# Kernel optimization log

Hardware: AMD Instinct MI355X
Metric: run time of the kernel (lower is better)

## Reference

```python
import jax, jax.numpy as jnp
import numpy as np

D_IN = 1024
D_OUT = 1024
H = 16            # head_cnt
G = 4             # attention_groups
LF = 2            # linformer_factor
HEAD_OUT = D_OUT // H          # 64 (value head dim)
DQ = HEAD_OUT // LF            # 32 (query/key head dim)
B, T = 2, 2048


def setup_inputs() -> dict:
    key = jax.random.key(0)
    ks = jax.random.split(key, 7)
    s = 0.02
    return {
        "x": jax.random.normal(ks[0], (B, T, D_IN), dtype=jnp.float32),
        "Wq": jax.random.normal(ks[1], (D_IN, D_OUT // LF), dtype=jnp.float32) * s,
        "Wk": jax.random.normal(ks[2], (D_IN, (D_OUT // LF) // G), dtype=jnp.float32) * s,
        "Wv": jax.random.normal(ks[3], (D_IN, D_OUT // G), dtype=jnp.float32) * s,
        "Wp": jax.random.normal(ks[4], (D_OUT, D_OUT), dtype=jnp.float32) * s,
        "bp": jnp.zeros((D_OUT,), dtype=jnp.float32),
    }


def _alibi_bias(T, dtype):
    # standard ALiBi slopes for H heads (H is a power of 2): m_h = 2^(-8h/H), h=1..H
    slopes = jnp.asarray(2.0 ** (-8.0 * np.arange(1, H + 1) / H), dtype=dtype)
    pos = jnp.arange(T)
    rel = (pos[None, :] - pos[:, None]).astype(dtype)  # j - i, <= 0 on causal part
    return slopes[:, None, None] * rel[None, :, :]      # (H, T, T)


def reference(x, Wq, Wk, Wv, Wp, bp):
    b, t, _ = x.shape
    q = x @ Wq                                  # (b, t, D_OUT/LF)
    k = jnp.tile(x @ Wk, (1, 1, G))             # repeat KV groups -> (b, t, D_OUT/LF)
    v = jnp.tile(x @ Wv, (1, 1, G))             # (b, t, D_OUT)

    q = q.reshape(b, t, H, DQ).transpose(0, 2, 1, 3)        # (b, H, t, DQ)
    k = k.reshape(b, t, H, DQ).transpose(0, 2, 1, 3)
    v = v.reshape(b, t, H, HEAD_OUT).transpose(0, 2, 1, 3)  # (b, H, t, HEAD_OUT)

    scores = jnp.einsum('bhqd,bhkd->bhqk', q, k)            # (b, H, t, t)
    causal = jnp.triu(jnp.ones((t, t), dtype=bool), k=1)
    scores = jnp.where(causal, -jnp.inf, scores)
    # faithful to source: alibi added after masking, then scaled by 1/sqrt(d_k)
    scores = (scores + _alibi_bias(t, scores.dtype)) / jnp.sqrt(jnp.asarray(DQ, scores.dtype))
    w = jax.nn.softmax(scores, axis=-1)
    ctx = jnp.einsum('bhqk,bhkd->bqhd', w, v).reshape(b, t, D_OUT)
    return ctx @ Wp + bp
```

## Files before the change

### kernel.cpp

```cpp
#include <hip/hip_runtime.h>
#include <hip/hip_bf16.h>

#define T_SEQ 2048
#define H_CNT 16
#define B_SZ  2
#define QKV_LD 896
#define KOFF   512
#define VOFF   640

typedef float  f32x4   __attribute__((ext_vector_type(4)));
typedef float  f32x16  __attribute__((ext_vector_type(16)));
typedef __bf16 bf16x8  __attribute__((ext_vector_type(8)));

static __device__ __forceinline__ ushort f2bf(float f) {
    union { float f; unsigned u; } v; v.f = f;
    unsigned u = v.u;
    unsigned r = (u + 0x7fffu + ((u >> 16) & 1u)) >> 16;
    return (ushort)r;
}
static __device__ __forceinline__ unsigned pack2bf(float a, float b) {
    union { __bf16 h[2]; unsigned u; } pk;
    pk.h[0] = (__bf16)a; pk.h[1] = (__bf16)b;
    return pk.u;
}

static __device__ __forceinline__ f32x4 mfma16(bf16x8 a, bf16x8 b, f32x4 c) {
    return __builtin_amdgcn_mfma_f32_16x16x32_bf16(a, b, c, 0, 0, 0);
}
static __device__ __forceinline__ f32x16 mfma32(bf16x8 a, bf16x8 b, f32x16 c) {
    return __builtin_amdgcn_mfma_f32_32x32x16_bf16(a, b, c, 0, 0, 0);
}

static __device__ __forceinline__ void gl_lds16(const void* g, void* l) {
    __builtin_amdgcn_global_load_lds((const __attribute__((address_space(1))) void*)g,
                                     (__attribute__((address_space(3))) void*)l, 16, 0, 0);
}

__global__ __launch_bounds__(256) void prep_inputs(const float* __restrict__ xin,
                                                   ushort* __restrict__ xb,
                                                   const float* __restrict__ Wq,
                                                   const float* __restrict__ Wk,
                                                   const float* __restrict__ Wv,
                                                   const float* __restrict__ Wp,
                                                   ushort* __restrict__ Wqkvt,
                                                   ushort* __restrict__ Wpt) {
    __shared__ float tile[32][33];
    const int n = blockIdx.x;
    if (n < 2048) {
        const int i = n * 256 + threadIdx.x;
        const float4 v0 = reinterpret_cast<const float4*>(xin)[i * 2];
        const float4 v1 = reinterpret_cast<const float4*>(xin)[i * 2 + 1];
        uint4 o;
        o.x = (unsigned)f2bf(v0.x) | ((unsigned)f2bf(v0.y) << 16);
        o.y = (unsigned)f2bf(v0.z) | ((unsigned)f2bf(v0.w) << 16);
        o.z = (unsigned)f2bf(v1.x) | ((unsigned)f2bf(v1.y) << 16);
        o.w = (unsigned)f2bf(v1.z) | ((unsigned)f2bf(v1.w) << 16);
        reinterpret_cast<uint4*>(xb)[i] = o;
        return;
    }
    const int m = n - 2048;
    const int x = m % 60;
    const int y = m / 60;
    const float* src; ushort* dst; int C, cx;
    if (x < 16)      { src = Wq; dst = Wqkvt;              C = 512;  cx = x; }
    else if (x < 20) { src = Wk; dst = Wqkvt + 512 * 1024; C = 128;  cx = x - 16; }
    else if (x < 28) { src = Wv; dst = Wqkvt + 640 * 1024; C = 256;  cx = x - 20; }
    else             { src = Wp; dst = Wpt;                C = 1024; cx = x - 28; }
    const int tx = threadIdx.x & 31, ty = threadIdx.x >> 5;
    const int r0 = y * 32, c0 = cx * 32;
#pragma unroll
    for (int i = 0; i < 32; i += 8)
        tile[ty + i][tx] = src[(size_t)(r0 + ty + i) * C + c0 + tx];
    __syncthreads();
#pragma unroll
    for (int i = 0; i < 32; i += 8)
        dst[(size_t)(c0 + ty + i) * 1024 + r0 + tx] = f2bf(tile[tx][ty + i]);
}

template <bool OUT_BF16, bool V_SPLIT>
__global__ __launch_bounds__(256) void gemm_bf16(const ushort* __restrict__ A,
                                                 const ushort* __restrict__ Bt,
                                                 const float* __restrict__ bias,
                                                 void* __restrict__ Cout,
                                                 ushort* __restrict__ vTb,
                                                 int M, int N, int K) {
    __shared__ __align__(16) ushort As[4][64 * 32];
    __shared__ __align__(16) ushort Bs[4][128 * 32];

    const int tid = threadIdx.x;
    const int w = tid >> 6, l = tid & 63;
    const int bm = blockIdx.y * 64, bn = blockIdx.x * 128;
    const int wr = (w >> 1) * 32, wc = (w & 1) * 64;
    const int lr = l & 15, lk = (l >> 4) * 8;
    const int crow = l >> 2, ck8 = (l & 3) * 8;

    const ushort* Ag  = A + (size_t)(bm + w * 16 + crow) * K + ck8;
    const ushort* Bg0 = Bt + (size_t)(bn + w * 16 + crow) * K + ck8;
    const ushort* Bg1 = Bt + (size_t)(bn + (w + 4) * 16 + crow) * K + ck8;

    f32x4 acc[2][4];
#pragma unroll
    for (int m = 0; m < 2; ++m)
#pragma unroll
        for (int n = 0; n < 4; ++n) acc[m][n] = (f32x4){0.f, 0.f, 0.f, 0.f};

    for (int k0 = 0; k0 < K; k0 += 128) {
        __syncthreads();
#pragma unroll
        for (int kk = 0; kk < 4; ++kk) {
            gl_lds16(Ag + k0 + kk * 32, &As[kk][w * 16 * 32]);
            gl_lds16(Bg0 + k0 + kk * 32, &Bs[kk][w * 16 * 32]);
            gl_lds16(Bg1 + k0 + kk * 32, &Bs[kk][(w + 4) * 16 * 32]);
        }
        __syncthreads();

#pragma unroll
        for (int kk = 0; kk < 4; ++kk) {
            bf16x8 af[2], bfr[4];
#pragma unroll
            for (int m = 0; m < 2; ++m)
                af[m] = *reinterpret_cast<const bf16x8*>(&As[kk][(wr + m * 16 + lr) * 32 + lk]);
#pragma unroll
            for (int n = 0; n < 4; ++n)
                bfr[n] = *reinterpret_cast<const bf16x8*>(&Bs[kk][(wc + n * 16 + lr) * 32 + lk]);
#pragma unroll
            for (int m = 0; m < 2; ++m)
#pragma unroll
                for (int n = 0; n < 4; ++n)
                    acc[m][n] = mfma16(af[m], bfr[n], acc[m][n]);
        }
    }

    const int orow = bm + wr + (l >> 4) * 4;
    const int ocol0 = bn + wc + lr;
#pragma unroll
    for (int m = 0; m < 2; ++m)
#pragma unroll
        for (int n = 0; n < 4; ++n) {
            const int col = ocol0 + n * 16;
            if (V_SPLIT && col >= VOFF) {
                uint2 pk;
                pk.x = (unsigned)f2bf(acc[m][n][0]) | ((unsigned)f2bf(acc[m][n][1]) << 16);
                pk.y = (unsigned)f2bf(acc[m][n][2]) | ((unsigned)f2bf(acc[m][n][3]) << 16);
                const int row0 = orow + m * 16;
                const size_t vidx = (size_t)(row0 >> 11) * 524288 +
                                    (size_t)(col - VOFF) * 2048 + (row0 & 2047);
                *reinterpret_cast<uint2*>(&vTb[vidx]) = pk;
                continue;
            }
            const float bv = OUT_BF16 ? 0.0f : bias[col];
#pragma unroll
            for (int r = 0; r < 4; ++r) {
                const size_t idx = (size_t)(orow + m * 16 + r) * N + col;
                if constexpr (OUT_BF16)
                    reinterpret_cast<ushort*>(Cout)[idx] = f2bf(acc[m][n][r]);
                else
                    reinterpret_cast<float*>(Cout)[idx] = acc[m][n][r] + bv;
            }
        }
}

#define LDK 40
#define LDV 136

__global__ __launch_bounds__(512) void attn_mfma9(const ushort* __restrict__ qkv,
                                                  const ushort* __restrict__ vT,
                                                  ushort* __restrict__ ctx) {
    __shared__ __align__(16) ushort Ks[2][128 * LDK];
    __shared__ __align__(16) ushort Vs[2][64 * LDV];
    __shared__ float lsred[4][32];

    const int tid = threadIdx.x;
    const int w = tid >> 6, l = tid & 63;
    const int lq = l & 31;
    const int hi = l >> 5;
    const int tp = blockIdx.x, g = blockIdx.y, b = blockIdx.z;
    const int hd = w & 3, grp = w >> 2;
    const int h = g + 4 * hd;

    const float slope = exp2f(-0.5f * (float)(h + 1));
    const float k1 = 0.17677669529663687f * 1.4426950408889634f;
    const float k2 = slope * k1;
    const int Wint = (int)(275.0f / slope);

    const int ksd = tid >> 2, kc4 = tid & 3;
    const ushort* kgp = qkv + (size_t)b * T_SEQ * QKV_LD + KOFF + g * 32 +
                        (size_t)ksd * QKV_LD + kc4 * 8;
    const int vsd = tid >> 3, vj = tid & 7;
    const int vs0 = (vj >> 2) << 1, vc4 = vj & 3;
    const int voff = (vc4 & 1) * 4 + (vc4 >> 1) * 16;
    const ushort* vgp = vT + ((size_t)b * 256 + g * 64 + vsd) * T_SEQ + vs0 * 32 + vc4 * 8;
    const int vl0 = vsd * LDV + vs0 * 32 + voff;
    const int vl1 = vsd * LDV + (vs0 + 1) * 32 + voff;

    float* red = reinterpret_cast<float*>(&Vs[0][0]);
    const int sidx = (hd * 64 + l) * 16;

    int cur = 0;
    for (int ph = 0; ph < 2; ++ph) {
        const int t = ph ? tp : (63 - tp);
        const int i0 = t * 32;
        const int nkeys = i0 + 32;
        const int jtmax = (nkeys + 127) & ~127;

        const ushort* qrow = qkv + ((size_t)(b * T_SEQ + i0 + lq)) * QKV_LD + h * 32 + hi * 8;
        const bf16x8 qa = *reinterpret_cast<const bf16x8*>(qrow);
        const bf16x8 qb = *reinterpret_cast<const bf16x8*>(qrow + 16);

        f32x16 o0, o1;
#pragma unroll
        for (int r = 0; r < 16; ++r) { o0[r] = 0.0f; o1[r] = 0.0f; }
        float ls = 0.0f;

        uint4 kreg, vr0, vr1;
        if (ksd < nkeys) kreg = *reinterpret_cast<const uint4*>(kgp);
        vr0 = *reinterpret_cast<const uint4*>(vgp);
        if (vs0 * 32 + 32 < nkeys) vr1 = *reinterpret_cast<const uint4*>(vgp + 32);

        for (int jt = 0; jt < jtmax; jt += 128) {
            *reinterpret_cast<uint4*>(&Ks[cur][ksd * LDK + kc4 * 8]) = kreg;
            *reinterpret_cast<uint2*>(&Vs[cur][vl0]) = make_uint2(vr0.x, vr0.y);
            *reinterpret_cast<uint2*>(&Vs[cur][vl0 + 8]) = make_uint2(vr0.z, vr0.w);
            *reinterpret_cast<uint2*>(&Vs[cur][vl1]) = make_uint2(vr1.x, vr1.y);
            *reinterpret_cast<uint2*>(&Vs[cur][vl1 + 8]) = make_uint2(vr1.z, vr1.w);
            const int jn = jt + 128;
            if (jn < jtmax) {
                if (jn + ksd < nkeys)
                    kreg = *reinterpret_cast<const uint4*>(kgp + (size_t)jn * QKV_LD);
                if (jn + vs0 * 32 < nkeys)
                    vr0 = *reinterpret_cast<const uint4*>(vgp + jn);
                if (jn + vs0 * 32 + 32 < nkeys)
                    vr1 = *reinterpret_cast<const uint4*>(vgp + jn + 32);
            }
            __syncthreads();

#pragma unroll
            for (int s = 0; s < 2; ++s) {
                const int si = s * 2 + grp;
                const int jts = jt + si * 32;
                if (jts < nkeys && jts + 31 >= i0 - Wint) {
                    const bf16x8 ka = *reinterpret_cast<const bf16x8*>(&Ks[cur][(si * 32 + lq) * LDK + hi * 8]);
                    const bf16x8 kb2 = *reinterpret_cast<const bf16x8*>(&Ks[cur][(si * 32 + lq) * LDK + 16 + hi * 8]);
                    f32x16 p;
#pragma unroll
                    for (int r = 0; r < 16; ++r) p[r] = 0.0f;
                    __builtin_amdgcn_s_setprio(1);
                    p = mfma32(ka, qa, p);
                    p = mfma32(kb2, qb, p);
                    __builtin_amdgcn_s_setprio(0);

                    const int dlt = jts + 4 * hi - i0 - lq;
                    const float base2 = k2 * (float)dlt;
                    float pe[16];
                    if (jts + 31 > i0) {
#pragma unroll
                        for (int r = 0; r < 16; ++r) {
                            const int off = (r & 3) + 8 * (r >> 2);
                            const float arg = fmaf(p[r], k1, fmaf((float)off, k2, base2));
                            float e = exp2f(arg);
                            if (dlt + off > 0) e = 0.0f;
                            ls += e;
                            pe[r] = e;
                        }
                    } else {
#pragma unroll
                        for (int r = 0; r < 16; ++r) {
                            const int off = (r & 3) + 8 * (r >> 2);
                            const float arg = fmaf(p[r], k1, fmaf((float)off, k2, base2));
                            const float e = exp2f(arg);
                            ls += e;
                            pe[r] = e;
                        }
                    }
                    union { unsigned u[4]; bf16x8 v; } A1, A2;
#pragma unroll
                    for (int j2 = 0; j2 < 4; ++j2) A1.u[j2] = pack2bf(pe[2 * j2], pe[2 * j2 + 1]);
#pragma unroll
                    for (int j2 = 0; j2 < 4; ++j2) A2.u[j2] = pack2bf(pe[8 + 2 * j2], pe[9 + 2 * j2]);

                    const int vr0i = lq * LDV + si * 32;
                    const int vr1i = (32 + lq) * LDV + si * 32;
                    const bf16x8 v00 = *reinterpret_cast<const bf16x8*>(&Vs[cur][vr0i + hi * 8]);
                    const bf16x8 v01 = *reinterpret_cast<const bf16x8*>(&Vs[cur][vr0i + 16 + hi * 8]);
                    const bf16x8 v10 = *reinterpret_cast<const bf16x8*>(&Vs[cur][vr1i + hi * 8]);
                    const bf16x8 v11 = *reinterpret_cast<const bf16x8*>(&Vs[cur][vr1i + 16 + hi * 8]);
                    __builtin_amdgcn_s_setprio(1);
                    o0 = mfma32(A1.v, v00, o0);
                    o0 = mfma32(A2.v, v01, o0);
                    o1 = mfma32(A1.v, v10, o1);
                    o1 = mfma32(A2.v, v11, o1);
                    __builtin_amdgcn_s_setprio(0);
                }
            }
            cur ^= 1;
        }

        const float ls2 = ls + __shfl_xor(ls, 32);
        __syncthreads();
        if (grp == 0) {
#pragma unroll
            for (int r = 0; r < 16; ++r) red[sidx + r] = o0[r];
            if (hi == 0) lsred[hd][lq] = ls2;
        }
        __syncthreads();
        float inv = 0.0f;
        if (grp == 1) {
#pragma unroll
            for (int r = 0; r < 16; ++r) o0[r] += red[sidx + r];
            inv = 1.0f / (ls2 + lsred[hd][lq]);
        }
        __syncthreads();
        if (grp == 0) {
#pragma unroll
            for (int r = 0; r < 16; ++r) red[sidx + r] = o1[r];
        }
        __syncthreads();
        if (grp == 1) {
#pragma unroll
            for (int r = 0; r < 16; ++r) o1[r] += red[sidx + r];
#pragma unroll
            for (int r = 0; r < 16; ++r) {
                const int qr = (r & 3) + 8 * (r >> 2) + 4 * hi;
                const float invq = __shfl(inv, qr);
                const size_t row = (size_t)(b * T_SEQ + i0 + qr);
                ctx[row * 1024 + h * 64 + lq] = f2bf(o0[r] * invq);
                ctx[row * 1024 + h * 64 + 32 + lq] = f2bf(o1[r] * invq);
            }
        }
        __syncthreads();
    }
}

extern "C" void kernel_launch(void* const* d_in, const int* in_sizes, int n_in,
                              void* d_out, int out_size, void* d_ws, size_t ws_size,
                              hipStream_t stream) {
    const float* x  = (const float*)d_in[0];
    const float* Wq = (const float*)d_in[1];
    const float* Wk = (const float*)d_in[2];
    const float* Wv = (const float*)d_in[3];
    const float* Wp = (const float*)d_in[4];
    const float* bp = (const float*)d_in[5];

    const int M = B_SZ * T_SEQ;

    ushort* ws    = (ushort*)d_ws;
    ushort* xb    = ws;
    ushort* Wqkvt = xb + 4194304;
    ushort* Wpt   = Wqkvt + 917504;
    ushort* qkv   = Wpt + 1048576;
    ushort* vTb   = qkv + 3670016;
    ushort* cbuf  = vTb + 1048576;

    prep_inputs<<<3968, 256, 0, stream>>>(x, xb, Wq, Wk, Wv, Wp, Wqkvt, Wpt);

    gemm_bf16<true, true><<<dim3(7, 64), 256, 0, stream>>>(
        xb, Wqkvt, nullptr, qkv, vTb, M, 896, 1024);

    attn_mfma9<<<dim3(32, 4, B_SZ), 512, 0, stream>>>(qkv, vTb, cbuf);

    gemm_bf16<false, false><<<dim3(8, 64), 256, 0, stream>>>(
        cbuf, Wpt, bp, (float*)d_out, nullptr, M, 1024, 1024);
}
```

Before: 83.59 us.

## Split attention key range across two blocks and combine partials in separate kernel

Replaces the paired-tile attention kernel (256 blocks each doing two query tiles) with a split-K style kernel of 1024 blocks, where each query tile's key tiles are divided into two halves. Each half writes unnormalized bf16 partial outputs and row sums, and a new combine kernel adds them and normalizes into the ctx buffer. This aims to raise parallelism and balance work across CUs on the causal workload. In exchange it adds a kernel launch, extra global traffic for the partial buffers, and bf16 rounding of the partial outputs.

```diff
diff --git a/kernel.cpp b/kernel.cpp
--- a/kernel.cpp
+++ b/kernel.cpp
@@ -17,6 +17,9 @@
     unsigned u = v.u;
     unsigned r = (u + 0x7fffu + ((u >> 16) & 1u)) >> 16;
     return (ushort)r;
+}
+static __device__ __forceinline__ float bf2f(unsigned x) {
+    union { unsigned u; float f; } v; v.u = x << 16; return v.f;
 }
 static __device__ __forceinline__ unsigned pack2bf(float a, float b) {
     union { __bf16 h[2]; unsigned u; } pk;
@@ -163,9 +166,10 @@
 #define LDK 40
 #define LDV 136
 
-__global__ __launch_bounds__(512) void attn_mfma9(const ushort* __restrict__ qkv,
-                                                  const ushort* __restrict__ vT,
-                                                  ushort* __restrict__ ctx) {
+__global__ __launch_bounds__(512) void attn_part(const ushort* __restrict__ qkv,
+                                                 const ushort* __restrict__ vT,
+                                                 ushort* __restrict__ part_o,
+                                                 float* __restrict__ part_l) {
     __shared__ __align__(16) ushort Ks[2][128 * LDK];
     __shared__ __align__(16) ushort Vs[2][64 * LDV];
     __shared__ float lsred[4][32];
@@ -174,9 +178,21 @@
     const int w = tid >> 6, l = tid & 63;
     const int lq = l & 31;
     const int hi = l >> 5;
-    const int tp = blockIdx.x, g = blockIdx.y, b = blockIdx.z;
+    const int m = blockIdx.x;
+    const int c = m & 255, rho = m >> 8;
+    const int g = c & 3, b = (c >> 2) & 1, j = c >> 3;
+    const int t = (rho & 1) ? (63 - j) : j;
+    const int half = rho >> 1;
+    const int i0 = t * 32;
     const int hd = w & 3, grp = w >> 2;
     const int h = g + 4 * hd;
+
+    const int nkeys = i0 + 32;
+    const int ntiles = (nkeys + 127) >> 7;
+    const int tiles0 = (ntiles + 1) >> 1;
+    const int itbeg = half ? tiles0 : 0;
+    const int itend = half ? ntiles : tiles0;
+    const int jt0 = itbeg * 128, jtend = itend * 128;
 
     const float slope = exp2f(-0.5f * (float)(h + 1));
     const float k1 = 0.17677669529663687f * 1.4426950408889634f;
@@ -196,138 +212,168 @@
     float* red = reinterpret_cast<float*>(&Vs[0][0]);
     const int sidx = (hd * 64 + l) * 16;
 
+    const ushort* qrow = qkv + ((size_t)(b * T_SEQ + i0 + lq)) * QKV_LD + h * 32 + hi * 8;
+    const bf16x8 qa = *reinterpret_cast<const bf16x8*>(qrow);
+    const bf16x8 qb = *reinterpret_cast<const bf16x8*>(qrow + 16);
+
+    f32x16 o0, o1;
+#pragma unroll
+    for (int r = 0; r < 16; ++r) { o0[r] = 0.0f; o1[r] = 0.0f; }
+    float ls = 0.0f;
+
+    uint4 kreg, vr0, vr1;
+    if (jt0 < jtend) {
+        if (jt0 + ksd < nkeys) kreg = *reinterpret_cast<const uint4*>(kgp + (size_t)jt0 * QKV_LD);
+        if (jt0 + vs0 * 32 < nkeys) vr0 = *reinterpret_cast<const uint4*>(vgp + jt0);
+        if (jt0 + vs0 * 32 + 32 < nkeys) vr1 = *reinterpret_cast<const uint4*>(vgp + jt0 + 32);
+    }
+
     int cur = 0;
-    for (int ph = 0; ph < 2; ++ph) {
-        const int t = ph ? tp : (63 - tp);
-        const int i0 = t * 32;
-        const int nkeys = i0 + 32;
-        const int jtmax = (nkeys + 127) & ~127;
-
-        const ushort* qrow = qkv + ((size_t)(b * T_SEQ + i0 + lq)) * QKV_LD + h * 32 + hi * 8;
-        const bf16x8 qa = *reinterpret_cast<const bf16x8*>(qrow);
-        const bf16x8 qb = *reinterpret_cast<const bf16x8*>(qrow + 16);
-
-        f32x16 o0, o1;
-#pragma unroll
-        for (int r = 0; r < 16; ++r) { o0[r] = 0.0f; o1[r] = 0.0f; }
-        float ls = 0.0f;
-
-        uint4 kreg, vr0, vr1;
-        if (ksd < nkeys) kreg = *reinterpret_cast<const uint4*>(kgp);
-        vr0 = *reinterpret_cast<const uint4*>(vgp);
-        if (vs0 * 32 + 32 < nkeys) vr1 = *reinterpret_cast<const uint4*>(vgp + 32);
-
-        for (int jt = 0; jt < jtmax; jt += 128) {
-            *reinterpret_cast<uint4*>(&Ks[cur][ksd * LDK + kc4 * 8]) = kreg;
-            *reinterpret_cast<uint2*>(&Vs[cur][vl0]) = make_uint2(vr0.x, vr0.y);
-            *reinterpret_cast<uint2*>(&Vs[cur][vl0 + 8]) = make_uint2(vr0.z, vr0.w);
-            *reinterpret_cast<uint2*>(&Vs[cur][vl1]) = make_uint2(vr1.x, vr1.y);
-            *reinterpret_cast<uint2*>(&Vs[cur][vl1 + 8]) = make_uint2(vr1.z, vr1.w);
-            const int jn = jt + 128;
-            if (jn < jtmax) {
-                if (jn + ksd < nkeys)
-                    kreg = *reinterpret_cast<const uint4*>(kgp + (size_t)jn * QKV_LD);
-                if (jn + vs0 * 32 < nkeys)
-                    vr0 = *reinterpret_cast<const uint4*>(vgp + jn);
-                if (jn + vs0 * 32 + 32 < nkeys)
-                    vr1 = *reinterpret_cast<const uint4*>(vgp + jn + 32);
+    for (int jt = jt0; jt < jtend; jt += 128) {
+        *reinterpret_cast<uint4*>(&Ks[cur][ksd * LDK + kc4 * 8]) = kreg;
+        *reinterpret_cast<uint2*>(&Vs[cur][vl0]) = make_uint2(vr0.x, vr0.y);
+        *reinterpret_cast<uint2*>(&Vs[cur][vl0 + 8]) = make_uint2(vr0.z, vr0.w);
+        *reinterpret_cast<uint2*>(&Vs[cur][vl1]) = make_uint2(vr1.x, vr1.y);
+        *reinterpret_cast<uint2*>(&Vs[cur][vl1 + 8]) = make_uint2(vr1.z, vr1.w);
+        const int jn = jt + 128;
+        if (jn < jtend) {
+            if (jn + ksd < nkeys)
+                kreg = *reinterpret_cast<const uint4*>(kgp + (size_t)jn * QKV_LD);
+            if (jn + vs0 * 32 < nkeys)
+                vr0 = *reinterpret_cast<const uint4*>(vgp + jn);
+            if (jn + vs0 * 32 + 32 < nkeys)
+                vr1 = *reinterpret_cast<const uint4*>(vgp + jn + 32);
+        }
+        __syncthreads();
+
+#pragma unroll
+        for (int s = 0; s < 2; ++s) {
+            const int si = s * 2 + grp;
+            const int jts = jt + si * 32;
+            if (jts < nkeys && jts + 31 >= i0 - Wint) {
+                const bf16x8 ka = *reinterpret_cast<const bf16x8*>(&Ks[cur][(si * 32 + lq) * LDK + hi * 8]);
+                const bf16x8 kb2 = *reinterpret_cast<const bf16x8*>(&Ks[cur][(si * 32 + lq) * LDK + 16 + hi * 8]);
+                f32x16 p;
+#pragma unroll
+                for (int r = 0; r < 16; ++r) p[r] = 0.0f;
+                __builtin_amdgcn_s_setprio(1);
+                p = mfma32(ka, qa, p);
+                p = mfma32(kb2, qb, p);
+                __builtin_amdgcn_s_setprio(0);
+
+                const int dlt = jts + 4 * hi - i0 - lq;
+                const float base2 = k2 * (float)dlt;
+                float pe[16];
+                if (jts + 31 > i0) {
+#pragma unroll
+                    for (int r = 0; r < 16; ++r) {
+                        const int off = (r & 3) + 8 * (r >> 2);
+                        const float arg = fmaf(p[r], k1, fmaf((float)off, k2, base2));
+                        float e = exp2f(arg);
+                        if (dlt + off > 0) e = 0.0f;
+                        ls += e;
+                        pe[r] = e;
+                    }
+                } else {
+#pragma unroll
+                    for (int r = 0; r < 16; ++r) {
+                        const int off = (r & 3) + 8 * (r >> 2);
+                        const float arg = fmaf(p[r], k1, fmaf((float)off, k2, base2));
+                        const float e = exp2f(arg);
+                        ls += e;
+                        pe[r] = e;
+                    }
+                }
+                union { unsigned u[4]; bf16x8 v; } A1, A2;
+#pragma unroll
+                for (int j2 = 0; j2 < 4; ++j2) A1.u[j2] = pack2bf(pe[2 * j2], pe[2 * j2 + 1]);
+#pragma unroll
+                for (int j2 = 0; j2 < 4; ++j2) A2.u[j2] = pack2bf(pe[8 + 2 * j2], pe[9 + 2 * j2]);
+
+                const int vr0i = lq * LDV + si * 32;
+                const int vr1i = (32 + lq) * LDV + si * 32;
+                const bf16x8 v00 = *reinterpret_cast<const bf16x8*>(&Vs[cur][vr0i + hi * 8]);
+                const bf16x8 v01 = *reinterpret_cast<const bf16x8*>(&Vs[cur][vr0i + 16 + hi * 8]);
+                const bf16x8 v10 = *reinterpret_cast<const bf16x8*>(&Vs[cur][vr1i + hi * 8]);
+                const bf16x8 v11 = *reinterpret_cast<const bf16x8*>(&Vs[cur][vr1i + 16 + hi * 8]);
+                __builtin_amdgcn_s_setprio(1);
+                o0 = mfma32(A1.v, v00, o0);
+                o0 = mfma32(A2.v, v01, o0);
+                o1 = mfma32(A1.v, v10, o1);
+                o1 = mfma32(A2.v, v11, o1);
+                __builtin_amdgcn_s_setprio(0);
             }
-            __syncthreads();
-
-#pragma unroll
-            for (int s = 0; s < 2; ++s) {
-                const int si = s * 2 + grp;
-                const int jts = jt + si * 32;
-                if (jts < nkeys && jts + 31 >= i0 - Wint) {
-                    const bf16x8 ka = *reinterpret_cast<const bf16x8*>(&Ks[cur][(si * 32 + lq) * LDK + hi * 8]);
-                    const bf16x8 kb2 = *reinterpret_cast<const bf16x8*>(&Ks[cur][(si * 32 + lq) * LDK + 16 + hi * 8]);
-                    f32x16 p;
-#pragma unroll
-                    for (int r = 0; r < 16; ++r) p[r] = 0.0f;
-                    __builtin_amdgcn_s_setprio(1);
-                    p = mfma32(ka, qa, p);
-                    p = mfma32(kb2, qb, p);
-                    __builtin_amdgcn_s_setprio(0);
-
-                    const int dlt = jts + 4 * hi - i0 - lq;
-                    const float base2 = k2 * (float)dlt;
-                    float pe[16];
-                    if (jts + 31 > i0) {
-#pragma unroll
-                        for (int r = 0; r < 16; ++r) {
-                            const int off = (r & 3) + 8 * (r >> 2);
-                            const float arg = fmaf(p[r], k1, fmaf((float)off, k2, base2));
-                            float e = exp2f(arg);
-                            if (dlt + off > 0) e = 0.0f;
-                            ls += e;
-                            pe[r] = e;
-                        }
-                    } else {
-#pragma unroll
-                        for (int r = 0; r < 16; ++r) {
-                            const int off = (r & 3) + 8 * (r >> 2);
-                            const float arg = fmaf(p[r], k1, fmaf((float)off, k2, base2));
-                            const float e = exp2f(arg);
-                            ls += e;
-                            pe[r] = e;
-                        }
-                    }
-                    union { unsigned u[4]; bf16x8 v; } A1, A2;
-#pragma unroll
-                    for (int j2 = 0; j2 < 4; ++j2) A1.u[j2] = pack2bf(pe[2 * j2], pe[2 * j2 + 1]);
-#pragma unroll
-                    for (int j2 = 0; j2 < 4; ++j2) A2.u[j2] = pack2bf(pe[8 + 2 * j2], pe[9 + 2 * j2]);
-
-                    const int vr0i = lq * LDV + si * 32;
-                    const int vr1i = (32 + lq) * LDV + si * 32;
-                    const bf16x8 v00 = *reinterpret_cast<const bf16x8*>(&Vs[cur][vr0i + hi * 8]);
-                    const bf16x8 v01 = *reinterpret_cast<const bf16x8*>(&Vs[cur][vr0i + 16 + hi * 8]);
-                    const bf16x8 v10 = *reinterpret_cast<const bf16x8*>(&Vs[cur][vr1i + hi * 8]);
-                    const bf16x8 v11 = *reinterpret_cast<const bf16x8*>(&Vs[cur][vr1i + 16 + hi * 8]);
-                    __builtin_amdgcn_s_setprio(1);
-                    o0 = mfma32(A1.v, v00, o0);
-                    o0 = mfma32(A2.v, v01, o0);
-                    o1 = mfma32(A1.v, v10, o1);
-                    o1 = mfma32(A2.v, v11, o1);
-                    __builtin_amdgcn_s_setprio(0);
-                }
-            }
-            cur ^= 1;
-        }
-
-        const float ls2 = ls + __shfl_xor(ls, 32);
-        __syncthreads();
-        if (grp == 0) {
-#pragma unroll
-            for (int r = 0; r < 16; ++r) red[sidx + r] = o0[r];
-            if (hi == 0) lsred[hd][lq] = ls2;
-        }
-        __syncthreads();
-        float inv = 0.0f;
-        if (grp == 1) {
-#pragma unroll
-            for (int r = 0; r < 16; ++r) o0[r] += red[sidx + r];
-            inv = 1.0f / (ls2 + lsred[hd][lq]);
-        }
-        __syncthreads();
-        if (grp == 0) {
-#pragma unroll
-            for (int r = 0; r < 16; ++r) red[sidx + r] = o1[r];
-        }
-        __syncthreads();
-        if (grp == 1) {
-#pragma unroll
-            for (int r = 0; r < 16; ++r) o1[r] += red[sidx + r];
-#pragma unroll
-            for (int r = 0; r < 16; ++r) {
-                const int qr = (r & 3) + 8 * (r >> 2) + 4 * hi;
-                const float invq = __shfl(inv, qr);
-                const size_t row = (size_t)(b * T_SEQ + i0 + qr);
-                ctx[row * 1024 + h * 64 + lq] = f2bf(o0[r] * invq);
-                ctx[row * 1024 + h * 64 + 32 + lq] = f2bf(o1[r] * invq);
-            }
-        }
-        __syncthreads();
+        }
+        cur ^= 1;
+    }
+
+    const float ls2 = ls + __shfl_xor(ls, 32);
+    __syncthreads();
+    if (grp == 0) {
+#pragma unroll
+        for (int r = 0; r < 16; ++r) red[sidx + r] = o0[r];
+        if (hi == 0) lsred[hd][lq] = ls2;
+    }
+    __syncthreads();
+    float lst = 0.0f;
+    if (grp == 1) {
+#pragma unroll
+        for (int r = 0; r < 16; ++r) o0[r] += red[sidx + r];
+        lst = ls2 + lsred[hd][lq];
+    }
+    __syncthreads();
+    if (grp == 0) {
+#pragma unroll
+        for (int r = 0; r < 16; ++r) red[sidx + r] = o1[r];
+    }
+    __syncthreads();
+    if (grp == 1) {
+#pragma unroll
+        for (int r = 0; r < 16; ++r) o1[r] += red[sidx + r];
+        const int slot = t * 8 + g * 2 + b;
+        const int area = slot * 2 + half;
+        if (hi == 0) part_l[area * 128 + hd * 32 + lq] = lst;
+#pragma unroll
+        for (int r = 0; r < 16; ++r) {
+            const int qr = (r & 3) + 8 * (r >> 2) + 4 * hi;
+            const size_t base = ((size_t)(area * 4 + hd) * 32 + qr) * 64;
+            part_o[base + lq] = f2bf(o0[r]);
+            part_o[base + 32 + lq] = f2bf(o1[r]);
+        }
+    }
+}
+
+__global__ __launch_bounds__(256) void attn_combine(const ushort* __restrict__ part_o,
+                                                    const float* __restrict__ part_l,
+                                                    ushort* __restrict__ ctx) {
+    const int s = blockIdx.x;
+    const int t = s >> 3, g = (s >> 1) & 3, b = s & 1;
+    const int tid = threadIdx.x;
+    const int row = tid >> 1;
+    const int hd = row >> 5, q = row & 31;
+    const int dh = (tid & 1) * 32;
+    const int aA = s * 2, aB = s * 2 + 1;
+    const float inv = 1.0f / (part_l[aA * 128 + hd * 32 + q] +
+                              part_l[aB * 128 + hd * 32 + q]);
+    const size_t bA = ((size_t)(aA * 4 + hd) * 32 + q) * 64 + dh;
+    const size_t bB = ((size_t)(aB * 4 + hd) * 32 + q) * 64 + dh;
+    const int hfull = g + 4 * hd;
+    const size_t ob = ((size_t)(b * T_SEQ + t * 32 + q)) * 1024 + hfull * 64 + dh;
+#pragma unroll
+    for (int cc = 0; cc < 4; ++cc) {
+        const uint4 ua = *reinterpret_cast<const uint4*>(&part_o[bA + cc * 8]);
+        const uint4 ub = *reinterpret_cast<const uint4*>(&part_o[bB + cc * 8]);
+        uint4 uo;
+        const unsigned* pa = &ua.x;
+        const unsigned* pb = &ub.x;
+        unsigned* po = &uo.x;
+#pragma unroll
+        for (int e = 0; e < 4; ++e) {
+            const float f0 = (bf2f(pa[e] & 0xffffu) + bf2f(pb[e] & 0xffffu)) * inv;
+            const float f1 = (bf2f(pa[e] >> 16) + bf2f(pb[e] >> 16)) * inv;
+            po[e] = (unsigned)f2bf(f0) | ((unsigned)f2bf(f1) << 16);
+        }
+        *reinterpret_cast<uint4*>(&ctx[ob + cc * 8]) = uo;
     }
 }
 
@@ -350,13 +396,16 @@
     ushort* qkv   = Wpt + 1048576;
     ushort* vTb   = qkv + 3670016;
     ushort* cbuf  = vTb + 1048576;
+    ushort* parto = cbuf + 4194304;
+    float*  partl = (float*)(parto + 8388608);
 
     prep_inputs<<<3968, 256, 0, stream>>>(x, xb, Wq, Wk, Wv, Wp, Wqkvt, Wpt);
 
     gemm_bf16<true, true><<<dim3(7, 64), 256, 0, stream>>>(
         xb, Wqkvt, nullptr, qkv, vTb, M, 896, 1024);
 
-    attn_mfma9<<<dim3(32, 4, B_SZ), 512, 0, stream>>>(qkv, vTb, cbuf);
+    attn_part<<<1024, 512, 0, stream>>>(qkv, vTb, parto, partl);
+    attn_combine<<<512, 256, 0, stream>>>(parto, partl, cbuf);
 
     gemm_bf16<false, false><<<dim3(8, 64), 256, 0, stream>>>(
         cbuf, Wpt, bp, (float*)d_out, nullptr, M, 1024, 1024);
```

Result: slower. 96.37 us (+15.3%).
